# Optimization experiments

Measured on AMD Instinct MI355X. Metric: run time of the kernel, lower is better.

The kernel has to match this reference:

```python
import jax, jax.numpy as jnp
import numpy as np

N_NODES = 100000


def gcn_conv(x, W, b, src, dst, deg_inv_sqrt):
    # x: [N, Cin], W: [Cin, Cout]. PyG GCNConv: transform then normalized aggregate.
    h = x @ W  # [N, Cout]
    norm = deg_inv_sqrt[src] * deg_inv_sqrt[dst]  # [E']
    msg = h[src] * norm[:, None]  # gather + scale
    out = jax.ops.segment_sum(msg, dst, num_segments=N_NODES)
    return out + b


def setup_inputs() -> dict:
    key = jax.random.key(0)
    ks = jax.random.split(key, 8)
    C = 256
    E = 3200000
    x = jax.random.normal(ks[0], (N_NODES, C), dtype=jnp.float32)
    edge_index = jax.random.randint(ks[1], (2, E), 0, N_NODES, dtype=jnp.int64)
    s = 1.0 / np.sqrt(C)
    W1 = jax.random.uniform(ks[2], (C, C), jnp.float32, -s, s)
    b1 = jnp.zeros((C,), jnp.float32)
    W2 = jax.random.uniform(ks[3], (C, C), jnp.float32, -s, s)
    b2 = jnp.zeros((C,), jnp.float32)
    Wl = jax.random.uniform(ks[4], (C, 1), jnp.float32, -s, s)
    bl = jnp.zeros((1,), jnp.float32)
    return {"x": x, "edge_index": edge_index, "W1": W1, "b1": b1,
            "W2": W2, "b2": b2, "Wl": Wl, "bl": bl}


def reference(x, edge_index, W1, b1, W2, b2, Wl, bl):
    # add self-loops once (shared by both conv layers)
    loops = jnp.arange(N_NODES, dtype=edge_index.dtype)
    src = jnp.concatenate([edge_index[0], loops])
    dst = jnp.concatenate([edge_index[1], loops])
    # symmetric normalization: deg counts incoming edges incl. self-loops
    deg = jax.ops.segment_sum(jnp.ones_like(dst, dtype=x.dtype), dst,
                              num_segments=N_NODES)
    deg_inv_sqrt = jax.lax.rsqrt(deg)  # deg >= 1 due to self-loops
    h = jax.nn.relu(gcn_conv(x, W1, b1, src, dst, deg_inv_sqrt))
    h = jax.nn.relu(gcn_conv(h, W2, b2, src, dst, deg_inv_sqrt))
    return h @ Wl + bl  # [N, 1]
```

## Files before the change

kernel.cpp:

```cpp
#include <hip/hip_runtime.h>

#define NN 100000
#define CC 256
#define EE 3200000

typedef __attribute__((ext_vector_type(8))) short bf16x8;
typedef __attribute__((ext_vector_type(4))) float f32x4;
typedef __attribute__((ext_vector_type(4))) _Float16 f16x4;

__device__ __forceinline__ float4 f4add(float4 a, float4 b) {
  return make_float4(a.x + b.x, a.y + b.y, a.z + b.z, a.w + b.w);
}

__device__ __forceinline__ unsigned short f2bf(float f) {
  unsigned u = __float_as_uint(f);
  unsigned r = (u + 0x7fffu + ((u >> 16) & 1u)) >> 16;
  return (unsigned short)r;
}
__device__ __forceinline__ float bf2f(unsigned short h) {
  return __uint_as_float(((unsigned)h) << 16);
}

__global__ void k_deg(const int* __restrict__ dst, int* __restrict__ cnt, int n) {
  int i = blockIdx.x * blockDim.x + threadIdx.x;
  int stride = gridDim.x * blockDim.x;
  for (; i < n; i += stride) {
    unsigned d = (unsigned)dst[i];
    if (d < NN) atomicAdd(&cnt[d], 1);
  }
}

__global__ void k_dis(const int* __restrict__ cnt, float* __restrict__ dis, int n) {
  int i = blockIdx.x * blockDim.x + threadIdx.x;
  if (i < n) dis[i] = 1.0f / sqrtf((float)(cnt[i] + 1));
}

__global__ void k_scan_local(const int* __restrict__ cnt, int* __restrict__ offs,
                             int* __restrict__ bsum, int n) {
  __shared__ int wsum[16];
  int t = threadIdx.x;
  int idx = blockIdx.x * 1024 + t;
  int lane = t & 63, wv = t >> 6;
  int v = (idx < n) ? cnt[idx] : 0;
  int x = v;
#pragma unroll
  for (int d = 1; d < 64; d <<= 1) {
    int y = __shfl_up(x, d, 64);
    if (lane >= d) x += y;
  }
  if (lane == 63) wsum[wv] = x;
  __syncthreads();
  int wpre = 0, total = 0;
#pragma unroll
  for (int w = 0; w < 16; ++w) {
    int s = wsum[w];
    if (w < wv) wpre += s;
    total += s;
  }
  if (idx < n) offs[idx] = wpre + x - v;
  if (t == 0) bsum[blockIdx.x] = total;
}

__global__ void k_scan_bsum(const int* __restrict__ bsum, int* __restrict__ bbase, int nb) {
  __shared__ int wsum[2];
  int t = threadIdx.x;
  int lane = t & 63, wv = t >> 6;
  int v = (t < nb) ? bsum[t] : 0;
  int x = v;
#pragma unroll
  for (int d = 1; d < 64; d <<= 1) {
    int y = __shfl_up(x, d, 64);
    if (lane >= d) x += y;
  }
  if (lane == 63) wsum[wv] = x;
  __syncthreads();
  int pre = (wv == 1) ? wsum[0] : 0;
  if (t < nb) bbase[t] = pre + x - v;
  if (t == nb - 1) bbase[nb] = pre + x;
}

__global__ void k_scan_add(int* __restrict__ offs, const int* __restrict__ bbase,
                           int n, int nb) {
  int i = blockIdx.x * 256 + threadIdx.x;
  if (i < n) offs[i] += bbase[i >> 10];
  if (i == 0) offs[n] = bbase[nb];
}

__global__ void k_scatter(const int* __restrict__ src, const int* __restrict__ dst,
                          const int* __restrict__ offs, int* __restrict__ fill,
                          int* __restrict__ csr, int n) {
  int i = blockIdx.x * blockDim.x + threadIdx.x;
  int stride = gridDim.x * blockDim.x;
  for (; i < n; i += stride) {
    unsigned d = (unsigned)dst[i];
    unsigned s = (unsigned)src[i];
    if (d < NN && s < NN) {
      int p = offs[d] + atomicAdd(&fill[d], 1);
      csr[p] = (int)s;
    }
  }
}

__global__ void k_wsplit(const float* __restrict__ W, unsigned short* __restrict__ WTh,
                         unsigned short* __restrict__ WTl) {
  int k = blockIdx.x, n = threadIdx.x;
  float w = W[k * CC + n];
  unsigned short h = f2bf(w);
  unsigned short l = f2bf(w - bf2f(h));
  WTh[n * CC + k] = h;
  WTl[n * CC + k] = l;
}

#define LDA 40

__global__ __launch_bounds__(512) void k_gemm_mfma(
    const float* __restrict__ A, const unsigned short* __restrict__ WTh,
    const unsigned short* __restrict__ WTl, const float* __restrict__ dis,
    _Float16* __restrict__ Out, int M) {
  __shared__ unsigned short Ah[128 * LDA], Al[128 * LDA];
  __shared__ unsigned short Bh[256 * LDA], Bl[256 * LDA];
  const int tid = threadIdx.x;
  const int wave = tid >> 6, lane = tid & 63;
  const int quad = lane >> 4, l16 = lane & 15;
  const int wm = wave >> 2, wn = wave & 3;
  const int row0 = blockIdx.x * 128;

  f32x4 acc[4][4];
#pragma unroll
  for (int i = 0; i < 4; ++i)
#pragma unroll
    for (int j = 0; j < 4; ++j) acc[i][j] = (f32x4){0.f, 0.f, 0.f, 0.f};

  for (int k0 = 0; k0 < CC; k0 += 32) {
#pragma unroll
    for (int q = 0; q < 2; ++q) {
      int idx = tid + 512 * q;
      int r = idx >> 3;
      int c4 = (idx & 7) << 2;
      int gr = row0 + r;
      float4 v = make_float4(0.f, 0.f, 0.f, 0.f);
      if (gr < M) v = *(const float4*)&A[(size_t)gr * CC + k0 + c4];
      ushort4 hv, lv;
      hv.x = f2bf(v.x); lv.x = f2bf(v.x - bf2f(hv.x));
      hv.y = f2bf(v.y); lv.y = f2bf(v.y - bf2f(hv.y));
      hv.z = f2bf(v.z); lv.z = f2bf(v.z - bf2f(hv.z));
      hv.w = f2bf(v.w); lv.w = f2bf(v.w - bf2f(hv.w));
      *(ushort4*)&Ah[r * LDA + c4] = hv;
      *(ushort4*)&Al[r * LDA + c4] = lv;
    }
#pragma unroll
    for (int q = 0; q < 4; ++q) {
      int idx = tid + 512 * q;
      int r = idx >> 3;
      int c4 = (idx & 7) << 2;
      const size_t g = (size_t)r * CC + k0 + c4;
      *(ushort4*)&Bh[r * LDA + c4] = *(const ushort4*)&WTh[g];
      *(ushort4*)&Bl[r * LDA + c4] = *(const ushort4*)&WTl[g];
    }
    __syncthreads();

    bf16x8 bh[4], bl[4];
#pragma unroll
    for (int j = 0; j < 4; ++j) {
      int br = (wn * 64 + j * 16 + l16) * LDA + quad * 8;
      bh[j] = *(const bf16x8*)&Bh[br];
      bl[j] = *(const bf16x8*)&Bl[br];
    }
#pragma unroll
    for (int i = 0; i < 4; ++i) {
      int ar = (wm * 64 + i * 16 + l16) * LDA + quad * 8;
      bf16x8 ah = *(const bf16x8*)&Ah[ar];
      bf16x8 al = *(const bf16x8*)&Al[ar];
#pragma unroll
      for (int j = 0; j < 4; ++j) {
        acc[i][j] = __builtin_amdgcn_mfma_f32_16x16x32_bf16(ah, bh[j], acc[i][j], 0, 0, 0);
        acc[i][j] = __builtin_amdgcn_mfma_f32_16x16x32_bf16(al, bh[j], acc[i][j], 0, 0, 0);
        acc[i][j] = __builtin_amdgcn_mfma_f32_16x16x32_bf16(ah, bl[j], acc[i][j], 0, 0, 0);
      }
    }
    __syncthreads();
  }

#pragma unroll
  for (int i = 0; i < 4; ++i) {
#pragma unroll
    for (int r4 = 0; r4 < 4; ++r4) {
      int r = row0 + wm * 64 + i * 16 + quad * 4 + r4;
      if (r < M) {
        float sc = dis[r];
#pragma unroll
        for (int j = 0; j < 4; ++j) {
          Out[(size_t)r * CC + wn * 64 + j * 16 + l16] =
              (_Float16)(acc[i][j][r4] * sc);
        }
      }
    }
  }
}

__global__ __launch_bounds__(256) void k_aggregate(
    const _Float16* __restrict__ hs, const int* __restrict__ offs,
    const int* __restrict__ csr, const float* __restrict__ dis,
    const float* __restrict__ bias, float* __restrict__ out, int n) {
  int node = blockIdx.x * 4 + (threadIdx.x >> 6);
  if (node >= n) return;
  int lane = threadIdx.x & 63;
  int c4 = lane << 2;
  int beg = offs[node], end = offs[node + 1];
  f16x4 sv = *(const f16x4*)&hs[(size_t)node * CC + c4];
  float4 a0 = make_float4((float)sv.x, (float)sv.y, (float)sv.z, (float)sv.w);
  float4 a1 = make_float4(0.f, 0.f, 0.f, 0.f);
  float4 a2 = make_float4(0.f, 0.f, 0.f, 0.f);
  float4 a3 = make_float4(0.f, 0.f, 0.f, 0.f);
  int e = beg;
  for (; e + 4 <= end; e += 4) {
    int s0 = csr[e], s1 = csr[e + 1], s2 = csr[e + 2], s3 = csr[e + 3];
    f16x4 v0 = *(const f16x4*)&hs[(size_t)s0 * CC + c4];
    f16x4 v1 = *(const f16x4*)&hs[(size_t)s1 * CC + c4];
    f16x4 v2 = *(const f16x4*)&hs[(size_t)s2 * CC + c4];
    f16x4 v3 = *(const f16x4*)&hs[(size_t)s3 * CC + c4];
    a0.x += (float)v0.x; a0.y += (float)v0.y; a0.z += (float)v0.z; a0.w += (float)v0.w;
    a1.x += (float)v1.x; a1.y += (float)v1.y; a1.z += (float)v1.z; a1.w += (float)v1.w;
    a2.x += (float)v2.x; a2.y += (float)v2.y; a2.z += (float)v2.z; a2.w += (float)v2.w;
    a3.x += (float)v3.x; a3.y += (float)v3.y; a3.z += (float)v3.z; a3.w += (float)v3.w;
  }
  for (; e < end; ++e) {
    int s0 = csr[e];
    f16x4 v0 = *(const f16x4*)&hs[(size_t)s0 * CC + c4];
    a0.x += (float)v0.x; a0.y += (float)v0.y; a0.z += (float)v0.z; a0.w += (float)v0.w;
  }
  float4 acc = f4add(f4add(a0, a1), f4add(a2, a3));
  float sc = dis[node];
  float4 bv = *(const float4*)&bias[c4];
  float4 r;
  r.x = fmaxf(acc.x * sc + bv.x, 0.f);
  r.y = fmaxf(acc.y * sc + bv.y, 0.f);
  r.z = fmaxf(acc.z * sc + bv.z, 0.f);
  r.w = fmaxf(acc.w * sc + bv.w, 0.f);
  *(float4*)&out[(size_t)node * CC + c4] = r;
}

__global__ __launch_bounds__(256) void k_aggregate_final(
    const _Float16* __restrict__ hs, const int* __restrict__ offs,
    const int* __restrict__ csr, const float* __restrict__ dis,
    const float* __restrict__ bias, const float* __restrict__ Wl,
    const float* __restrict__ bl, float* __restrict__ out, int n) {
  int node = blockIdx.x * 4 + (threadIdx.x >> 6);
  if (node >= n) return;
  int lane = threadIdx.x & 63;
  int c4 = lane << 2;
  int beg = offs[node], end = offs[node + 1];
  f16x4 sv = *(const f16x4*)&hs[(size_t)node * CC + c4];
  float4 a0 = make_float4((float)sv.x, (float)sv.y, (float)sv.z, (float)sv.w);
  float4 a1 = make_float4(0.f, 0.f, 0.f, 0.f);
  float4 a2 = make_float4(0.f, 0.f, 0.f, 0.f);
  float4 a3 = make_float4(0.f, 0.f, 0.f, 0.f);
  int e = beg;
  for (; e + 4 <= end; e += 4) {
    int s0 = csr[e], s1 = csr[e + 1], s2 = csr[e + 2], s3 = csr[e + 3];
    f16x4 v0 = *(const f16x4*)&hs[(size_t)s0 * CC + c4];
    f16x4 v1 = *(const f16x4*)&hs[(size_t)s1 * CC + c4];
    f16x4 v2 = *(const f16x4*)&hs[(size_t)s2 * CC + c4];
    f16x4 v3 = *(const f16x4*)&hs[(size_t)s3 * CC + c4];
    a0.x += (float)v0.x; a0.y += (float)v0.y; a0.z += (float)v0.z; a0.w += (float)v0.w;
    a1.x += (float)v1.x; a1.y += (float)v1.y; a1.z += (float)v1.z; a1.w += (float)v1.w;
    a2.x += (float)v2.x; a2.y += (float)v2.y; a2.z += (float)v2.z; a2.w += (float)v2.w;
    a3.x += (float)v3.x; a3.y += (float)v3.y; a3.z += (float)v3.z; a3.w += (float)v3.w;
  }
  for (; e < end; ++e) {
    int s0 = csr[e];
    f16x4 v0 = *(const f16x4*)&hs[(size_t)s0 * CC + c4];
    a0.x += (float)v0.x; a0.y += (float)v0.y; a0.z += (float)v0.z; a0.w += (float)v0.w;
  }
  float4 acc = f4add(f4add(a0, a1), f4add(a2, a3));
  float sc = dis[node];
  float4 bv = *(const float4*)&bias[c4];
  float4 w = *(const float4*)&Wl[c4];
  float s = fmaxf(acc.x * sc + bv.x, 0.f) * w.x +
            fmaxf(acc.y * sc + bv.y, 0.f) * w.y +
            fmaxf(acc.z * sc + bv.z, 0.f) * w.z +
            fmaxf(acc.w * sc + bv.w, 0.f) * w.w;
#pragma unroll
  for (int d = 32; d > 0; d >>= 1) s += __shfl_down(s, d, 64);
  if (lane == 0) out[node] = s + bl[0];
}

extern "C" void kernel_launch(void* const* d_in, const int* in_sizes, int n_in,
                              void* d_out, int out_size, void* d_ws, size_t ws_size,
                              hipStream_t stream) {
  const float* x = (const float*)d_in[0];
  const int* ei = (const int*)d_in[1];
  const float* W1 = (const float*)d_in[2];
  const float* b1 = (const float*)d_in[3];
  const float* W2 = (const float*)d_in[4];
  const float* b2 = (const float*)d_in[5];
  const float* Wl = (const float*)d_in[6];
  const float* bl = (const float*)d_in[7];
  float* out = (float*)d_out;

  const int* src = ei;
  const int* dst = ei + EE;

  char* ws = (char*)d_ws;
  size_t off = 0;
  auto alloc = [&](size_t bytes) {
    char* p = ws + off;
    off = (off + bytes + 255) & ~(size_t)255;
    return p;
  };
  float* dis = (float*)alloc((size_t)NN * 4);
  int* cnt = (int*)alloc((size_t)NN * 4);
  int* offs = (int*)alloc((size_t)(NN + 1) * 4);
  int* scanb = (int*)alloc(1024 * 4);
  int* scanb2 = (int*)alloc(1024 * 4);
  int* csr = (int*)alloc((size_t)EE * 4);
  unsigned short* W1h = (unsigned short*)alloc((size_t)CC * CC * 2);
  unsigned short* W1l = (unsigned short*)alloc((size_t)CC * CC * 2);
  unsigned short* W2h = (unsigned short*)alloc((size_t)CC * CC * 2);
  unsigned short* W2l = (unsigned short*)alloc((size_t)CC * CC * 2);
  _Float16* hsbuf = (_Float16*)alloc((size_t)NN * CC * 2);
  float* h1 = (float*)alloc((size_t)NN * CC * 4);

  hipMemsetAsync(cnt, 0, (size_t)NN * 4, stream);

  k_deg<<<2048, 256, 0, stream>>>(dst, cnt, EE);
  k_dis<<<(NN + 255) / 256, 256, 0, stream>>>(cnt, dis, NN);
  const int nb = (NN + 1023) / 1024;
  k_scan_local<<<nb, 1024, 0, stream>>>(cnt, offs, scanb, NN);
  k_scan_bsum<<<1, 128, 0, stream>>>(scanb, scanb2, nb);
  k_scan_add<<<(NN + 255) / 256, 256, 0, stream>>>(offs, scanb2, NN, nb);
  hipMemsetAsync(cnt, 0, (size_t)NN * 4, stream);
  k_scatter<<<2048, 256, 0, stream>>>(src, dst, offs, cnt, csr, EE);

  k_wsplit<<<CC, CC, 0, stream>>>(W1, W1h, W1l);
  k_wsplit<<<CC, CC, 0, stream>>>(W2, W2h, W2l);

  const int gblocks = (NN + 127) / 128;
  k_gemm_mfma<<<gblocks, 512, 0, stream>>>(x, W1h, W1l, dis, hsbuf, NN);
  k_aggregate<<<(NN + 3) / 4, 256, 0, stream>>>(hsbuf, offs, csr, dis, b1, h1, NN);
  k_gemm_mfma<<<gblocks, 512, 0, stream>>>(h1, W2h, W2l, dis, hsbuf, NN);
  k_aggregate_final<<<(NN + 3) / 4, 256, 0, stream>>>(hsbuf, offs, csr, dis, b2, Wl, bl, out, NN);
}
```

Measured before the change: 1.057 ms.

## Fuse CSR setup into one cooperative kernel and widen aggregate gather unroll

Replaces the degree count, normalisation, three-stage scan, memsets, scatter and weight-split launches with a single cooperative kernel that uses grid-wide syncs, removing about ten launches and their gaps. The aggregation loops are unrolled from 4 to 8 edges per iteration to keep more gathers in flight. The setup kernel runs on only 256 blocks of 256 threads, so the atomic-heavy degree and scatter passes get less parallelism, and each grid sync adds latency.

```diff
diff --git a/kernel.cpp b/kernel.cpp
--- a/kernel.cpp
+++ b/kernel.cpp
@@ -1,8 +1,15 @@
 #include <hip/hip_runtime.h>
+#include <hip/hip_cooperative_groups.h>
+
+namespace cg = cooperative_groups;
 
 #define NN 100000
 #define CC 256
 #define EE 3200000
+
+#define SB 256
+#define ST 256
+#define CHUNK 391
 
 typedef __attribute__((ext_vector_type(8))) short bf16x8;
 typedef __attribute__((ext_vector_type(4))) float f32x4;
@@ -21,94 +28,112 @@
   return __uint_as_float(((unsigned)h) << 16);
 }
 
-__global__ void k_deg(const int* __restrict__ dst, int* __restrict__ cnt, int n) {
-  int i = blockIdx.x * blockDim.x + threadIdx.x;
-  int stride = gridDim.x * blockDim.x;
-  for (; i < n; i += stride) {
+__global__ void k_setup(const int* __restrict__ src, const int* __restrict__ dst,
+                        const float* __restrict__ W1, const float* __restrict__ W2,
+                        int* __restrict__ cnt, float* __restrict__ dis,
+                        int* __restrict__ offs, int* __restrict__ bsum,
+                        int* __restrict__ bbase,
+                        unsigned short* __restrict__ W1h, unsigned short* __restrict__ W1l,
+                        unsigned short* __restrict__ W2h, unsigned short* __restrict__ W2l,
+                        int* __restrict__ csr) {
+  cg::grid_group grid = cg::this_grid();
+  const int tid = threadIdx.x;
+  const int b = blockIdx.x;
+  const int gtid = b * ST + tid;
+  const int nthr = SB * ST;
+  const int lane = tid & 63, wv = tid >> 6;
+  __shared__ int sh_w[4];
+
+  for (int i = gtid; i < NN; i += nthr) cnt[i] = 0;
+  {
+    int k = gtid >> 8, n = gtid & 255;
+    float w1 = W1[k * CC + n];
+    unsigned short h1 = f2bf(w1);
+    W1h[n * CC + k] = h1;
+    W1l[n * CC + k] = f2bf(w1 - bf2f(h1));
+    float w2 = W2[k * CC + n];
+    unsigned short h2 = f2bf(w2);
+    W2h[n * CC + k] = h2;
+    W2l[n * CC + k] = f2bf(w2 - bf2f(h2));
+  }
+  grid.sync();
+
+  for (int i = gtid; i < EE; i += nthr) {
     unsigned d = (unsigned)dst[i];
     if (d < NN) atomicAdd(&cnt[d], 1);
   }
-}
-
-__global__ void k_dis(const int* __restrict__ cnt, float* __restrict__ dis, int n) {
-  int i = blockIdx.x * blockDim.x + threadIdx.x;
-  if (i < n) dis[i] = 1.0f / sqrtf((float)(cnt[i] + 1));
-}
-
-__global__ void k_scan_local(const int* __restrict__ cnt, int* __restrict__ offs,
-                             int* __restrict__ bsum, int n) {
-  __shared__ int wsum[16];
-  int t = threadIdx.x;
-  int idx = blockIdx.x * 1024 + t;
-  int lane = t & 63, wv = t >> 6;
-  int v = (idx < n) ? cnt[idx] : 0;
-  int x = v;
-#pragma unroll
-  for (int d = 1; d < 64; d <<= 1) {
-    int y = __shfl_up(x, d, 64);
-    if (lane >= d) x += y;
-  }
-  if (lane == 63) wsum[wv] = x;
-  __syncthreads();
-  int wpre = 0, total = 0;
-#pragma unroll
-  for (int w = 0; w < 16; ++w) {
-    int s = wsum[w];
-    if (w < wv) wpre += s;
-    total += s;
-  }
-  if (idx < n) offs[idx] = wpre + x - v;
-  if (t == 0) bsum[blockIdx.x] = total;
-}
-
-__global__ void k_scan_bsum(const int* __restrict__ bsum, int* __restrict__ bbase, int nb) {
-  __shared__ int wsum[2];
-  int t = threadIdx.x;
-  int lane = t & 63, wv = t >> 6;
-  int v = (t < nb) ? bsum[t] : 0;
-  int x = v;
-#pragma unroll
-  for (int d = 1; d < 64; d <<= 1) {
-    int y = __shfl_up(x, d, 64);
-    if (lane >= d) x += y;
-  }
-  if (lane == 63) wsum[wv] = x;
-  __syncthreads();
-  int pre = (wv == 1) ? wsum[0] : 0;
-  if (t < nb) bbase[t] = pre + x - v;
-  if (t == nb - 1) bbase[nb] = pre + x;
-}
-
-__global__ void k_scan_add(int* __restrict__ offs, const int* __restrict__ bbase,
-                           int n, int nb) {
-  int i = blockIdx.x * 256 + threadIdx.x;
-  if (i < n) offs[i] += bbase[i >> 10];
-  if (i == 0) offs[n] = bbase[nb];
-}
-
-__global__ void k_scatter(const int* __restrict__ src, const int* __restrict__ dst,
-                          const int* __restrict__ offs, int* __restrict__ fill,
-                          int* __restrict__ csr, int n) {
-  int i = blockIdx.x * blockDim.x + threadIdx.x;
-  int stride = gridDim.x * blockDim.x;
-  for (; i < n; i += stride) {
+  grid.sync();
+
+  const int c0 = b * CHUNK;
+  const int c1e = (c0 + CHUNK < NN) ? c0 + CHUNK : NN;
+  int lsum = 0;
+  for (int i = c0 + tid; i < c1e; i += ST) {
+    int c = cnt[i];
+    lsum += c;
+    dis[i] = 1.0f / sqrtf((float)(c + 1));
+  }
+  {
+    int x = lsum;
+#pragma unroll
+    for (int d = 32; d > 0; d >>= 1) x += __shfl_down(x, d, 64);
+    if (lane == 0) sh_w[wv] = x;
+    __syncthreads();
+    if (tid == 0) bsum[b] = sh_w[0] + sh_w[1] + sh_w[2] + sh_w[3];
+  }
+  grid.sync();
+
+  if (b == 0) {
+    __syncthreads();
+    int v = bsum[tid];
+    int x = v;
+#pragma unroll
+    for (int d = 1; d < 64; d <<= 1) {
+      int y = __shfl_up(x, d, 64);
+      if (lane >= d) x += y;
+    }
+    if (lane == 63) sh_w[wv] = x;
+    __syncthreads();
+    int pre = 0;
+#pragma unroll
+    for (int w = 0; w < 4; ++w)
+      if (w < wv) pre += sh_w[w];
+    bbase[tid] = pre + x - v;
+    if (tid == 255) bbase[SB] = pre + x;
+  }
+  grid.sync();
+
+  {
+    __syncthreads();
+    int i0 = c0 + 2 * tid, i1 = i0 + 1;
+    int v0 = (i0 < c1e) ? cnt[i0] : 0;
+    int v1 = (i1 < c1e) ? cnt[i1] : 0;
+    int p = v0 + v1, x = p;
+#pragma unroll
+    for (int d = 1; d < 64; d <<= 1) {
+      int y = __shfl_up(x, d, 64);
+      if (lane >= d) x += y;
+    }
+    if (lane == 63) sh_w[wv] = x;
+    __syncthreads();
+    int pre = 0;
+#pragma unroll
+    for (int w = 0; w < 4; ++w)
+      if (w < wv) pre += sh_w[w];
+    int base = bbase[b] + pre + x - p;
+    if (i0 < c1e) { offs[i0] = base; cnt[i0] = 0; }
+    if (i1 < c1e) { offs[i1] = base + v0; cnt[i1] = 0; }
+    if (gtid == 0) offs[NN] = bbase[SB];
+  }
+  grid.sync();
+
+  for (int i = gtid; i < EE; i += nthr) {
     unsigned d = (unsigned)dst[i];
     unsigned s = (unsigned)src[i];
     if (d < NN && s < NN) {
-      int p = offs[d] + atomicAdd(&fill[d], 1);
+      int p = offs[d] + atomicAdd(&cnt[d], 1);
       csr[p] = (int)s;
     }
   }
-}
-
-__global__ void k_wsplit(const float* __restrict__ W, unsigned short* __restrict__ WTh,
-                         unsigned short* __restrict__ WTl) {
-  int k = blockIdx.x, n = threadIdx.x;
-  float w = W[k * CC + n];
-  unsigned short h = f2bf(w);
-  unsigned short l = f2bf(w - bf2f(h));
-  WTh[n * CC + k] = h;
-  WTl[n * CC + k] = l;
 }
 
 #define LDA 40
@@ -213,18 +238,34 @@
   float4 a2 = make_float4(0.f, 0.f, 0.f, 0.f);
   float4 a3 = make_float4(0.f, 0.f, 0.f, 0.f);
   int e = beg;
-  for (; e + 4 <= end; e += 4) {
-    int s0 = csr[e], s1 = csr[e + 1], s2 = csr[e + 2], s3 = csr[e + 3];
+  for (; e + 8 <= end; e += 8) {
+    int s0 = csr[e],     s1 = csr[e + 1], s2 = csr[e + 2], s3 = csr[e + 3];
+    int s4 = csr[e + 4], s5 = csr[e + 5], s6 = csr[e + 6], s7 = csr[e + 7];
     f16x4 v0 = *(const f16x4*)&hs[(size_t)s0 * CC + c4];
     f16x4 v1 = *(const f16x4*)&hs[(size_t)s1 * CC + c4];
     f16x4 v2 = *(const f16x4*)&hs[(size_t)s2 * CC + c4];
     f16x4 v3 = *(const f16x4*)&hs[(size_t)s3 * CC + c4];
+    f16x4 v4 = *(const f16x4*)&hs[(size_t)s4 * CC + c4];
+    f16x4 v5 = *(const f16x4*)&hs[(size_t)s5 * CC + c4];
+    f16x4 v6 = *(const f16x4*)&hs[(size_t)s6 * CC + c4];
+    f16x4 v7 = *(const f16x4*)&hs[(size_t)s7 * CC + c4];
+    a0.x += (float)v0.x + (float)v4.x; a0.y += (float)v0.y + (float)v4.y;
+    a0.z += (float)v0.z + (float)v4.z; a0.w += (float)v0.w + (float)v4.w;
+    a1.x += (float)v1.x + (float)v5.x; a1.y += (float)v1.y + (float)v5.y;
+    a1.z += (float)v1.z + (float)v5.z; a1.w += (float)v1.w + (float)v5.w;
+    a2.x += (float)v2.x + (float)v6.x; a2.y += (float)v2.y + (float)v6.y;
+    a2.z += (float)v2.z + (float)v6.z; a2.w += (float)v2.w + (float)v6.w;
+    a3.x += (float)v3.x + (float)v7.x; a3.y += (float)v3.y + (float)v7.y;
+    a3.z += (float)v3.z + (float)v7.z; a3.w += (float)v3.w + (float)v7.w;
+  }
+  for (; e + 2 <= end; e += 2) {
+    int s0 = csr[e], s1 = csr[e + 1];
+    f16x4 v0 = *(const f16x4*)&hs[(size_t)s0 * CC + c4];
+    f16x4 v1 = *(const f16x4*)&hs[(size_t)s1 * CC + c4];
     a0.x += (float)v0.x; a0.y += (float)v0.y; a0.z += (float)v0.z; a0.w += (float)v0.w;
     a1.x += (float)v1.x; a1.y += (float)v1.y; a1.z += (float)v1.z; a1.w += (float)v1.w;
-    a2.x += (float)v2.x; a2.y += (float)v2.y; a2.z += (float)v2.z; a2.w += (float)v2.w;
-    a3.x += (float)v3.x; a3.y += (float)v3.y; a3.z += (float)v3.z; a3.w += (float)v3.w;
-  }
-  for (; e < end; ++e) {
+  }
+  if (e < end) {
     int s0 = csr[e];
     f16x4 v0 = *(const f16x4*)&hs[(size_t)s0 * CC + c4];
     a0.x += (float)v0.x; a0.y += (float)v0.y; a0.z += (float)v0.z; a0.w += (float)v0.w;
@@ -256,18 +297,34 @@
   float4 a2 = make_float4(0.f, 0.f, 0.f, 0.f);
   float4 a3 = make_float4(0.f, 0.f, 0.f, 0.f);
   int e = beg;
-  for (; e + 4 <= end; e += 4) {
-    int s0 = csr[e], s1 = csr[e + 1], s2 = csr[e + 2], s3 = csr[e + 3];
+  for (; e + 8 <= end; e += 8) {
+    int s0 = csr[e],     s1 = csr[e + 1], s2 = csr[e + 2], s3 = csr[e + 3];
+    int s4 = csr[e + 4], s5 = csr[e + 5], s6 = csr[e + 6], s7 = csr[e + 7];
     f16x4 v0 = *(const f16x4*)&hs[(size_t)s0 * CC + c4];
     f16x4 v1 = *(const f16x4*)&hs[(size_t)s1 * CC + c4];
     f16x4 v2 = *(const f16x4*)&hs[(size_t)s2 * CC + c4];
     f16x4 v3 = *(const f16x4*)&hs[(size_t)s3 * CC + c4];
+    f16x4 v4 = *(const f16x4*)&hs[(size_t)s4 * CC + c4];
+    f16x4 v5 = *(const f16x4*)&hs[(size_t)s5 * CC + c4];
+    f16x4 v6 = *(const f16x4*)&hs[(size_t)s6 * CC + c4];
+    f16x4 v7 = *(const f16x4*)&hs[(size_t)s7 * CC + c4];
+    a0.x += (float)v0.x + (float)v4.x; a0.y += (float)v0.y + (float)v4.y;
+    a0.z += (float)v0.z + (float)v4.z; a0.w += (float)v0.w + (float)v4.w;
+    a1.x += (float)v1.x + (float)v5.x; a1.y += (float)v1.y + (float)v5.y;
+    a1.z += (float)v1.z + (float)v5.z; a1.w += (float)v1.w + (float)v5.w;
+    a2.x += (float)v2.x + (float)v6.x; a2.y += (float)v2.y + (float)v6.y;
+    a2.z += (float)v2.z + (float)v6.z; a2.w += (float)v2.w + (float)v6.w;
+    a3.x += (float)v3.x + (float)v7.x; a3.y += (float)v3.y + (float)v7.y;
+    a3.z += (float)v3.z + (float)v7.z; a3.w += (float)v3.w + (float)v7.w;
+  }
+  for (; e + 2 <= end; e += 2) {
+    int s0 = csr[e], s1 = csr[e + 1];
+    f16x4 v0 = *(const f16x4*)&hs[(size_t)s0 * CC + c4];
+    f16x4 v1 = *(const f16x4*)&hs[(size_t)s1 * CC + c4];
     a0.x += (float)v0.x; a0.y += (float)v0.y; a0.z += (float)v0.z; a0.w += (float)v0.w;
     a1.x += (float)v1.x; a1.y += (float)v1.y; a1.z += (float)v1.z; a1.w += (float)v1.w;
-    a2.x += (float)v2.x; a2.y += (float)v2.y; a2.z += (float)v2.z; a2.w += (float)v2.w;
-    a3.x += (float)v3.x; a3.y += (float)v3.y; a3.z += (float)v3.z; a3.w += (float)v3.w;
-  }
-  for (; e < end; ++e) {
+  }
+  if (e < end) {
     int s0 = csr[e];
     f16x4 v0 = *(const f16x4*)&hs[(size_t)s0 * CC + c4];
     a0.x += (float)v0.x; a0.y += (float)v0.y; a0.z += (float)v0.z; a0.w += (float)v0.w;
@@ -298,8 +355,8 @@
   const float* bl = (const float*)d_in[7];
   float* out = (float*)d_out;
 
-  const int* src = ei;
-  const int* dst = ei + EE;
+  const int* srcp = ei;
+  const int* dstp = ei + EE;
 
   char* ws = (char*)d_ws;
   size_t off = 0;
@@ -311,8 +368,8 @@
   float* dis = (float*)alloc((size_t)NN * 4);
   int* cnt = (int*)alloc((size_t)NN * 4);
   int* offs = (int*)alloc((size_t)(NN + 1) * 4);
-  int* scanb = (int*)alloc(1024 * 4);
-  int* scanb2 = (int*)alloc(1024 * 4);
+  int* bsum = (int*)alloc(1024 * 4);
+  int* bbase = (int*)alloc(1024 * 4);
   int* csr = (int*)alloc((size_t)EE * 4);
   unsigned short* W1h = (unsigned short*)alloc((size_t)CC * CC * 2);
   unsigned short* W1l = (unsigned short*)alloc((size_t)CC * CC * 2);
@@ -321,19 +378,14 @@
   _Float16* hsbuf = (_Float16*)alloc((size_t)NN * CC * 2);
   float* h1 = (float*)alloc((size_t)NN * CC * 4);
 
-  hipMemsetAsync(cnt, 0, (size_t)NN * 4, stream);
-
-  k_deg<<<2048, 256, 0, stream>>>(dst, cnt, EE);
-  k_dis<<<(NN + 255) / 256, 256, 0, stream>>>(cnt, dis, NN);
-  const int nb = (NN + 1023) / 1024;
-  k_scan_local<<<nb, 1024, 0, stream>>>(cnt, offs, scanb, NN);
-  k_scan_bsum<<<1, 128, 0, stream>>>(scanb, scanb2, nb);
-  k_scan_add<<<(NN + 255) / 256, 256, 0, stream>>>(offs, scanb2, NN, nb);
-  hipMemsetAsync(cnt, 0, (size_t)NN * 4, stream);
-  k_scatter<<<2048, 256, 0, stream>>>(src, dst, offs, cnt, csr, EE);
-
-  k_wsplit<<<CC, CC, 0, stream>>>(W1, W1h, W1l);
-  k_wsplit<<<CC, CC, 0, stream>>>(W2, W2h, W2l);
+  {
+    void* args[] = {(void*)&srcp, (void*)&dstp, (void*)&W1, (void*)&W2,
+                    (void*)&cnt, (void*)&dis, (void*)&offs, (void*)&bsum,
+                    (void*)&bbase, (void*)&W1h, (void*)&W1l, (void*)&W2h,
+                    (void*)&W2l, (void*)&csr};
+    hipLaunchCooperativeKernel((const void*)k_setup, dim3(SB), dim3(ST),
+                               args, 0, stream);
+  }
 
   const int gblocks = (NN + 127) / 128;
   k_gemm_mfma<<<gblocks, 512, 0, stream>>>(x, W1h, W1l, dis, hsbuf, NN);
```

Result: slower. 1.201 ms (+13.6%).
